# Kernel optimization log

Measured on AMD Instinct MI355X. Metric: run time of the kernel, lower is better.

Reference implementation:

```python
import jax, jax.numpy as jnp
import numpy as np

OUT_F = 4096
IN_F = 4096
NUM_BITS = 4
BLOCK = 64
R = 16
LORA_SCALE = 32.0 / R  # lora_alpha / r


def setup_inputs() -> dict:
    key = jax.random.key(0)
    k1, k2, k3, k4, k5, k6 = jax.random.split(key, 6)
    n_packed = OUT_F * IN_F * NUM_BITS // 8  # bytes; 2 nibbles per byte
    n_blocks = OUT_F * IN_F // BLOCK
    return {
        "x": jax.random.normal(k1, (2, 1024, IN_F), dtype=jnp.float32),
        "qweight": jax.random.randint(k2, (n_packed,), 0, 256, dtype=jnp.int32),
        "scales": jax.random.uniform(k3, (n_blocks,), dtype=jnp.float32),
        "bias": jax.random.normal(k4, (OUT_F,), dtype=jnp.float32),
        "lora_A": jax.random.normal(k5, (R, IN_F), dtype=jnp.float32) * 0.02,
        "lora_B": jax.random.normal(k6, (OUT_F, R), dtype=jnp.float32) * 0.02,
    }


def _dequantize(qweight, scales):
    # uniform 4-bit lookup table: linspace(-1, 1, 16)
    table = jnp.linspace(-1.0, 1.0, 2 ** NUM_BITS).astype(scales.dtype)
    mask = (1 << NUM_BITS) - 1
    # unpack: index i stored at bits [i*NUM_BITS, (i+1)*NUM_BITS) of each byte
    lo = qweight & mask
    hi = (qweight >> NUM_BITS) & mask
    idx = jnp.stack([lo, hi], axis=-1).reshape(-1)  # [OUT_F*IN_F]
    vals = table[idx]                                # gather from lookup table
    # per-block rescale, then reshape to [OUT_F, IN_F]
    w = vals.reshape(-1, BLOCK) * scales[:, None]
    return w.reshape(OUT_F, IN_F)


def reference(x, qweight, scales, bias, lora_A, lora_B):
    W = _dequantize(qweight, scales)                      # [out, in]
    base = jnp.einsum('bsi,oi->bso', x, W) + bias          # F.linear
    lora = jnp.einsum('bsr,or->bso', jnp.einsum('bsi,ri->bsr', x, lora_A), lora_B)
    return base + LORA_SCALE * lora
```

## Files before the change

### kernel.cpp

```cpp
#include <hip/hip_runtime.h>
#include <hip/hip_bf16.h>
#include <stdint.h>

#define IN_F   4096
#define OUT_F  4096
#define M_ROWS 2048
#define LORA_SCALE 2.0f

typedef __bf16 bf16x8 __attribute__((ext_vector_type(8)));
typedef float  f32x4  __attribute__((ext_vector_type(4)));

typedef const __attribute__((address_space(1))) void gvoid_t;
typedef __attribute__((address_space(3))) void lvoid_t;

__global__ void dequant_kernel(const int* __restrict__ qw,
                               const float* __restrict__ scales,
                               __hip_bfloat16* __restrict__ W) {
    int t = blockIdx.x * 256 + threadIdx.x;
    int4 q = ((const int4*)qw)[t];
    float scale = scales[t >> 3];
    float step = scale * (2.0f / 15.0f);
    int b[4] = {q.x, q.y, q.z, q.w};
    union { __hip_bfloat16 h[8]; uint4 v; } o;
    #pragma unroll
    for (int j = 0; j < 4; ++j) {
        float lo = (float)(b[j] & 15)        * step - scale;
        float hi = (float)((b[j] >> 4) & 15) * step - scale;
        o.h[2*j]   = __float2bfloat16(lo);
        o.h[2*j+1] = __float2bfloat16(hi);
    }
    ((uint4*)W)[t] = o.v;
}

__global__ void xcast_kernel(const float* __restrict__ x,
                             __hip_bfloat16* __restrict__ xb) {
    int t = blockIdx.x * 256 + threadIdx.x;
    float4 a = ((const float4*)x)[2*t];
    float4 b = ((const float4*)x)[2*t + 1];
    union { __hip_bfloat16 h[8]; uint4 v; } o;
    o.h[0] = __float2bfloat16(a.x); o.h[1] = __float2bfloat16(a.y);
    o.h[2] = __float2bfloat16(a.z); o.h[3] = __float2bfloat16(a.w);
    o.h[4] = __float2bfloat16(b.x); o.h[5] = __float2bfloat16(b.y);
    o.h[6] = __float2bfloat16(b.z); o.h[7] = __float2bfloat16(b.w);
    ((uint4*)xb)[t] = o.v;
}

__global__ void lora_t_kernel(const float* __restrict__ x,
                              const float* __restrict__ A,
                              float* __restrict__ tout) {
    __shared__ float red[16 * 4 * 16];
    int m0 = blockIdx.x * 4;
    int r = threadIdx.x & 15;
    int g = threadIdx.x >> 4;
    float acc[4] = {0.f, 0.f, 0.f, 0.f};
    for (int kb = 0; kb < 64; ++kb) {
        int k = kb * 64 + g * 4;
        float4 av = *(const float4*)(A + (size_t)r * IN_F + k);
        #pragma unroll
        for (int row = 0; row < 4; ++row) {
            float4 xv = *(const float4*)(x + (size_t)(m0 + row) * IN_F + k);
            acc[row] += xv.x*av.x + xv.y*av.y + xv.z*av.z + xv.w*av.w;
        }
    }
    #pragma unroll
    for (int row = 0; row < 4; ++row) red[g*64 + row*16 + r] = acc[row];
    __syncthreads();
    if (threadIdx.x < 64) {
        int row = threadIdx.x >> 4, rr = threadIdx.x & 15;
        float s = 0.f;
        #pragma unroll
        for (int gg = 0; gg < 16; ++gg) s += red[gg*64 + row*16 + rr];
        tout[(size_t)(m0 + row) * 16 + rr] = s;
    }
}

__global__ __launch_bounds__(256) void gemm_kernel(
        const __hip_bfloat16* __restrict__ A,
        const __hip_bfloat16* __restrict__ B,
        const float* __restrict__ bias,
        const float* __restrict__ loraB,
        const float* __restrict__ tmat,
        float* __restrict__ out) {
    const int K = IN_F, N = OUT_F;
    __shared__ union alignas(16) {
        struct { __hip_bfloat16 As[128*32]; __hip_bfloat16 Bs[128*32]; } s;
        float tstage[128 * 16];
    } sm;

    int tid  = threadIdx.x;
    int wave = tid >> 6, lane = tid & 63;
    int wm = wave >> 1, wn = wave & 1;
    int row16 = lane & 15, quad = lane >> 4;
    int m0 = blockIdx.y * 128, n0 = blockIdx.x * 128;

    int srow = lane >> 2;
    int scol = (lane & 3) * 8;

    f32x4 acc[4][4];
    #pragma unroll
    for (int i = 0; i < 4; ++i)
        #pragma unroll
        for (int j = 0; j < 4; ++j) acc[i][j] = (f32x4){0.f, 0.f, 0.f, 0.f};

    const __hip_bfloat16* Abase = A + (size_t)m0 * K;
    const __hip_bfloat16* Bbase = B + (size_t)n0 * K;

    for (int k0 = 0; k0 < K; k0 += 32) {
        #pragma unroll
        for (int j = 0; j < 2; ++j) {
            int seg = wave * 2 + j;
            const __hip_bfloat16* gA = Abase + (size_t)(seg*16 + srow) * K + k0 + scol;
            __builtin_amdgcn_global_load_lds((gvoid_t*)gA,
                (lvoid_t*)&sm.s.As[seg * 512], 16, 0, 0);
            const __hip_bfloat16* gB = Bbase + (size_t)(seg*16 + srow) * K + k0 + scol;
            __builtin_amdgcn_global_load_lds((gvoid_t*)gB,
                (lvoid_t*)&sm.s.Bs[seg * 512], 16, 0, 0);
        }
        __syncthreads();

        bf16x8 af[4], bfr[4];
        #pragma unroll
        for (int mt = 0; mt < 4; ++mt)
            af[mt] = *(const bf16x8*)&sm.s.As[(wm*64 + mt*16 + row16)*32 + quad*8];
        #pragma unroll
        for (int nt = 0; nt < 4; ++nt)
            bfr[nt] = *(const bf16x8*)&sm.s.Bs[(wn*64 + nt*16 + row16)*32 + quad*8];
        #pragma unroll
        for (int mt = 0; mt < 4; ++mt)
            #pragma unroll
            for (int nt = 0; nt < 4; ++nt)
                acc[mt][nt] = __builtin_amdgcn_mfma_f32_16x16x32_bf16(
                    af[mt], bfr[nt], acc[mt][nt], 0, 0, 0);
        __syncthreads();
    }

    for (int i = tid; i < 512; i += 256)
        ((float4*)sm.tstage)[i] = ((const float4*)(tmat + (size_t)m0 * 16))[i];
    __syncthreads();

    #pragma unroll
    for (int nt = 0; nt < 4; ++nt) {
        int nl = wn*64 + nt*16 + row16;
        int n  = n0 + nl;
        float bn = bias[n];
        const float4* lb = (const float4*)(loraB + (size_t)n * 16);
        float4 lb0 = lb[0], lb1 = lb[1], lb2 = lb[2], lb3 = lb[3];
        #pragma unroll
        for (int mt = 0; mt < 4; ++mt) {
            #pragma unroll
            for (int r = 0; r < 4; ++r) {
                int ml = wm*64 + mt*16 + quad*4 + r;
                const float* tm = &sm.tstage[ml * 16];
                float dot =
                    tm[0]*lb0.x + tm[1]*lb0.y + tm[2]*lb0.z + tm[3]*lb0.w +
                    tm[4]*lb1.x + tm[5]*lb1.y + tm[6]*lb1.z + tm[7]*lb1.w +
                    tm[8]*lb2.x + tm[9]*lb2.y + tm[10]*lb2.z + tm[11]*lb2.w +
                    tm[12]*lb3.x + tm[13]*lb3.y + tm[14]*lb3.z + tm[15]*lb3.w;
                out[(size_t)(m0 + ml) * N + n] = acc[mt][nt][r] + bn + LORA_SCALE * dot;
            }
        }
    }
}

extern "C" void kernel_launch(void* const* d_in, const int* in_sizes, int n_in,
                              void* d_out, int out_size, void* d_ws, size_t ws_size,
                              hipStream_t stream) {
    const float* x      = (const float*)d_in[0];
    const int*   qw     = (const int*)d_in[1];
    const float* scales = (const float*)d_in[2];
    const float* bias   = (const float*)d_in[3];
    const float* loraA  = (const float*)d_in[4];
    const float* loraB  = (const float*)d_in[5];
    float* out = (float*)d_out;

    char* ws = (char*)d_ws;
    __hip_bfloat16* Wb = (__hip_bfloat16*)ws;
    __hip_bfloat16* Xb = (__hip_bfloat16*)(ws + 33554432);
    float* tmat        = (float*)(ws + 33554432 + 16777216);

    dequant_kernel<<<8192, 256, 0, stream>>>(qw, scales, Wb);
    xcast_kernel  <<<4096, 256, 0, stream>>>(x, Xb);
    lora_t_kernel <<<512,  256, 0, stream>>>(x, loraA, tmat);
    gemm_kernel   <<<dim3(32, 16), 256, 0, stream>>>(Xb, Wb, bias, loraB, tmat, out);
}
```

Before: 325.8 us.

## Double-buffer GEMM LDS tiles with 512-thread blocks and merge prep kernels

Fuses the dequantize and x-cast kernels into one launch that picks its branch by block index. The GEMM now uses 512 threads (8 waves, each owning a 32x64 sub-tile) and double-buffers the A/B LDS tiles, issuing the next k-slice's global-to-LDS load before computing on the current one. This keeps one barrier per iteration. The aim is to overlap memory latency with MFMA work and cut launch overhead, at the cost of doubled LDS use and a higher launch-bounds occupancy target.

```diff
diff --git a/kernel.cpp b/kernel.cpp
--- a/kernel.cpp
+++ b/kernel.cpp
@@ -13,36 +13,38 @@
 typedef const __attribute__((address_space(1))) void gvoid_t;
 typedef __attribute__((address_space(3))) void lvoid_t;
 
-__global__ void dequant_kernel(const int* __restrict__ qw,
-                               const float* __restrict__ scales,
-                               __hip_bfloat16* __restrict__ W) {
-    int t = blockIdx.x * 256 + threadIdx.x;
-    int4 q = ((const int4*)qw)[t];
-    float scale = scales[t >> 3];
-    float step = scale * (2.0f / 15.0f);
-    int b[4] = {q.x, q.y, q.z, q.w};
-    union { __hip_bfloat16 h[8]; uint4 v; } o;
-    #pragma unroll
-    for (int j = 0; j < 4; ++j) {
-        float lo = (float)(b[j] & 15)        * step - scale;
-        float hi = (float)((b[j] >> 4) & 15) * step - scale;
-        o.h[2*j]   = __float2bfloat16(lo);
-        o.h[2*j+1] = __float2bfloat16(hi);
+__global__ void prep_kernel(const int* __restrict__ qw,
+                            const float* __restrict__ scales,
+                            __hip_bfloat16* __restrict__ W,
+                            const float* __restrict__ x,
+                            __hip_bfloat16* __restrict__ xb) {
+    int b = blockIdx.x;
+    if (b < 8192) {
+        int t = b * 256 + threadIdx.x;
+        int4 q = ((const int4*)qw)[t];
+        float scale = scales[t >> 3];
+        float step = scale * (2.0f / 15.0f);
+        int bb[4] = {q.x, q.y, q.z, q.w};
+        union { __hip_bfloat16 h[8]; uint4 v; } o;
+        #pragma unroll
+        for (int j = 0; j < 4; ++j) {
+            float lo = (float)(bb[j] & 15)        * step - scale;
+            float hi = (float)((bb[j] >> 4) & 15) * step - scale;
+            o.h[2*j]   = __float2bfloat16(lo);
+            o.h[2*j+1] = __float2bfloat16(hi);
+        }
+        ((uint4*)W)[t] = o.v;
+    } else {
+        int t = (b - 8192) * 256 + threadIdx.x;
+        float4 a = ((const float4*)x)[2*t];
+        float4 c = ((const float4*)x)[2*t + 1];
+        union { __hip_bfloat16 h[8]; uint4 v; } o;
+        o.h[0] = __float2bfloat16(a.x); o.h[1] = __float2bfloat16(a.y);
+        o.h[2] = __float2bfloat16(a.z); o.h[3] = __float2bfloat16(a.w);
+        o.h[4] = __float2bfloat16(c.x); o.h[5] = __float2bfloat16(c.y);
+        o.h[6] = __float2bfloat16(c.z); o.h[7] = __float2bfloat16(c.w);
+        ((uint4*)xb)[t] = o.v;
     }
-    ((uint4*)W)[t] = o.v;
-}
-
-__global__ void xcast_kernel(const float* __restrict__ x,
-                             __hip_bfloat16* __restrict__ xb) {
-    int t = blockIdx.x * 256 + threadIdx.x;
-    float4 a = ((const float4*)x)[2*t];
-    float4 b = ((const float4*)x)[2*t + 1];
-    union { __hip_bfloat16 h[8]; uint4 v; } o;
-    o.h[0] = __float2bfloat16(a.x); o.h[1] = __float2bfloat16(a.y);
-    o.h[2] = __float2bfloat16(a.z); o.h[3] = __float2bfloat16(a.w);
-    o.h[4] = __float2bfloat16(b.x); o.h[5] = __float2bfloat16(b.y);
-    o.h[6] = __float2bfloat16(b.z); o.h[7] = __float2bfloat16(b.w);
-    ((uint4*)xb)[t] = o.v;
 }
 
 __global__ void lora_t_kernel(const float* __restrict__ x,
@@ -74,7 +76,7 @@
     }
 }
 
-__global__ __launch_bounds__(256) void gemm_kernel(
+__global__ __launch_bounds__(512, 4) void gemm_kernel(
         const __hip_bfloat16* __restrict__ A,
         const __hip_bfloat16* __restrict__ B,
         const float* __restrict__ bias,
@@ -83,7 +85,7 @@
         float* __restrict__ out) {
     const int K = IN_F, N = OUT_F;
     __shared__ union alignas(16) {
-        struct { __hip_bfloat16 As[128*32]; __hip_bfloat16 Bs[128*32]; } s;
+        struct { __hip_bfloat16 As[2][128*32]; __hip_bfloat16 Bs[2][128*32]; } s;
         float tstage[128 * 16];
     } sm;
 
@@ -96,46 +98,46 @@
     int srow = lane >> 2;
     int scol = (lane & 3) * 8;
 
-    f32x4 acc[4][4];
+    const __hip_bfloat16* gA0 = A + (size_t)(m0 + wave*16 + srow) * K + scol;
+    const __hip_bfloat16* gB0 = B + (size_t)(n0 + wave*16 + srow) * K + scol;
+
+    f32x4 acc[2][4];
     #pragma unroll
-    for (int i = 0; i < 4; ++i)
+    for (int i = 0; i < 2; ++i)
         #pragma unroll
         for (int j = 0; j < 4; ++j) acc[i][j] = (f32x4){0.f, 0.f, 0.f, 0.f};
 
-    const __hip_bfloat16* Abase = A + (size_t)m0 * K;
-    const __hip_bfloat16* Bbase = B + (size_t)n0 * K;
+    __builtin_amdgcn_global_load_lds((gvoid_t*)gA0, (lvoid_t*)&sm.s.As[0][wave*512], 16, 0, 0);
+    __builtin_amdgcn_global_load_lds((gvoid_t*)gB0, (lvoid_t*)&sm.s.Bs[0][wave*512], 16, 0, 0);
+    __syncthreads();
 
     for (int k0 = 0; k0 < K; k0 += 32) {
+        int cur = (k0 >> 5) & 1;
+        if (k0 + 32 < K) {
+            __builtin_amdgcn_global_load_lds((gvoid_t*)(gA0 + k0 + 32),
+                (lvoid_t*)&sm.s.As[cur^1][wave*512], 16, 0, 0);
+            __builtin_amdgcn_global_load_lds((gvoid_t*)(gB0 + k0 + 32),
+                (lvoid_t*)&sm.s.Bs[cur^1][wave*512], 16, 0, 0);
+        }
+
+        bf16x8 af[2], bfr[4];
         #pragma unroll
-        for (int j = 0; j < 2; ++j) {
-            int seg = wave * 2 + j;
-            const __hip_bfloat16* gA = Abase + (size_t)(seg*16 + srow) * K + k0 + scol;
-            __builtin_amdgcn_global_load_lds((gvoid_t*)gA,
-                (lvoid_t*)&sm.s.As[seg * 512], 16, 0, 0);
-            const __hip_bfloat16* gB = Bbase + (size_t)(seg*16 + srow) * K + k0 + scol;
-            __builtin_amdgcn_global_load_lds((gvoid_t*)gB,
-                (lvoid_t*)&sm.s.Bs[seg * 512], 16, 0, 0);
-        }
-        __syncthreads();
-
-        bf16x8 af[4], bfr[4];
-        #pragma unroll
-        for (int mt = 0; mt < 4; ++mt)
-            af[mt] = *(const bf16x8*)&sm.s.As[(wm*64 + mt*16 + row16)*32 + quad*8];
+        for (int mt = 0; mt < 2; ++mt)
+            af[mt] = *(const bf16x8*)&sm.s.As[cur][(wm*32 + mt*16 + row16)*32 + quad*8];
         #pragma unroll
         for (int nt = 0; nt < 4; ++nt)
-            bfr[nt] = *(const bf16x8*)&sm.s.Bs[(wn*64 + nt*16 + row16)*32 + quad*8];
+            bfr[nt] = *(const bf16x8*)&sm.s.Bs[cur][(wn*64 + nt*16 + row16)*32 + quad*8];
         #pragma unroll
-        for (int mt = 0; mt < 4; ++mt)
+        for (int mt = 0; mt < 2; ++mt)
             #pragma unroll
             for (int nt = 0; nt < 4; ++nt)
                 acc[mt][nt] = __builtin_amdgcn_mfma_f32_16x16x32_bf16(
                     af[mt], bfr[nt], acc[mt][nt], 0, 0, 0);
+
         __syncthreads();
     }
 
-    for (int i = tid; i < 512; i += 256)
-        ((float4*)sm.tstage)[i] = ((const float4*)(tmat + (size_t)m0 * 16))[i];
+    ((float4*)sm.tstage)[tid] = ((const float4*)(tmat + (size_t)m0 * 16))[tid];
     __syncthreads();
 
     #pragma unroll
@@ -146,10 +148,10 @@
         const float4* lb = (const float4*)(loraB + (size_t)n * 16);
         float4 lb0 = lb[0], lb1 = lb[1], lb2 = lb[2], lb3 = lb[3];
         #pragma unroll
-        for (int mt = 0; mt < 4; ++mt) {
+        for (int mt = 0; mt < 2; ++mt) {
             #pragma unroll
             for (int r = 0; r < 4; ++r) {
-                int ml = wm*64 + mt*16 + quad*4 + r;
+                int ml = wm*32 + mt*16 + quad*4 + r;
                 const float* tm = &sm.tstage[ml * 16];
                 float dot =
                     tm[0]*lb0.x + tm[1]*lb0.y + tm[2]*lb0.z + tm[3]*lb0.w +
@@ -178,8 +180,7 @@
     __hip_bfloat16* Xb = (__hip_bfloat16*)(ws + 33554432);
     float* tmat        = (float*)(ws + 33554432 + 16777216);
 
-    dequant_kernel<<<8192, 256, 0, stream>>>(qw, scales, Wb);
-    xcast_kernel  <<<4096, 256, 0, stream>>>(x, Xb);
-    lora_t_kernel <<<512,  256, 0, stream>>>(x, loraA, tmat);
-    gemm_kernel   <<<dim3(32, 16), 256, 0, stream>>>(Xb, Wb, bias, loraB, tmat, out);
+    prep_kernel  <<<12288, 256, 0, stream>>>(qw, scales, Wb, x, Xb);
+    lora_t_kernel<<<512,  256, 0, stream>>>(x, loraA, tmat);
+    gemm_kernel  <<<dim3(32, 16), 512, 0, stream>>>(Xb, Wb, bias, loraB, tmat, out);
 }
```

Result: slower. 355.9 us (+9.2%).
